# Kernel tuning notes

Measured on AMD Instinct MI355X. Metric: run time of the kernel, lower is better.

## Reference

```python
import jax, jax.numpy as jnp
import numpy as np
from jax import lax

HID = 768          # hidden_dim / embedding_dim
IN = 64            # input_dim = max_seq_length // num_heads
SEQ = 512          # max_seq_length
GROUPS = IN        # conv groups
BLUR_K = 5
BLUR_SIGMA = 1.0


def _gauss1d(k, sigma):
    half = (k - 1) * 0.5
    x = np.linspace(-half, half, k)
    pdf = np.exp(-0.5 * (x / sigma) ** 2)
    return pdf / pdf.sum()


def setup_inputs() -> dict:
    key = jax.random.key(0)
    ks = jax.random.split(key, 8)
    s = 0.02
    return {
        "inputs": jax.random.normal(ks[0], (16, SEQ, HID), jnp.float32),
        # Conv1d(768, 768, k=3, groups=64): weight [out_ch, in_ch/groups, k]
        "conv_w": jax.random.normal(ks[1], (HID, HID // GROUPS, 3), jnp.float32) * s,
        "conv_b": jnp.zeros((HID,), jnp.float32),
        "ln_g": jnp.ones((IN,), jnp.float32),
        "ln_b": jnp.zeros((IN,), jnp.float32),
        # function_info: Linear(64, 64), torch weight convention [out, in]
        "fi_w": jax.random.normal(ks[2], (IN, IN), jnp.float32) * s,
        "fi_b": jnp.zeros((IN,), jnp.float32),
        # block_info: Linear(64, 1)
        "bi_w": jax.random.normal(ks[3], (1, IN), jnp.float32) * s,
        "bi_b": jnp.zeros((1,), jnp.float32),
    }


def _forward(inputs, conv_w, conv_b, ln_g, ln_b, fi_w, fi_b, bi_w, bi_b):
    x = inputs.reshape(-1, HID, IN)  # [Bn, 768, 64] (raw row-major view, as torch .view)
    q = k = v = m = x

    # q: grouped Conv1d + residual, GELU, LayerNorm over last dim (64)
    qc = lax.conv_general_dilated(
        q, conv_w, window_strides=(1,), padding=[(1, 1)],
        feature_group_count=GROUPS, dimension_numbers=("NCH", "OIH", "NCH"))
    qc = qc + conv_b[None, :, None]
    q = jax.nn.gelu(qc + q, approximate=False)
    mu = jnp.mean(q, axis=-1, keepdims=True)
    var = jnp.mean(jnp.square(q - mu), axis=-1, keepdims=True)
    q = (q - mu) * lax.rsqrt(var + 1e-5) * ln_g + ln_b

    # v: Linear(64,64) + GELU
    v = jax.nn.gelu(v @ fi_w.T + fi_b, approximate=False)

    # k: dropout (eval -> identity), softmax over dim=-2 (channel axis), GELU
    k = jax.nn.gelu(jax.nn.softmax(k, axis=-2), approximate=False)

    # m: GaussianBlur(5, sigma fixed 1.0) over (H=768, W=64) with reflect pad, then Linear(64,1)
    g = _gauss1d(BLUR_K, BLUR_SIGMA)
    kern = jnp.asarray(np.outer(g, g), m.dtype)[None, None]  # [1,1,5,5]
    p = BLUR_K // 2
    mp = jnp.pad(m[:, None], ((0, 0), (0, 0), (p, p), (p, p)), mode="reflect")
    m = lax.conv_general_dilated(
        mp, kern, (1, 1), "VALID", dimension_numbers=("NCHW", "OIHW", "NCHW"))[:, 0]
    m = m @ bi_w.T + bi_b                        # [Bn, 768, 1]
    mask = jnp.broadcast_to(m, (m.shape[0], HID, HID))  # expand to [Bn,768,768]

    # SDPA: scale = 1/sqrt(E) with E = q.shape[-1] = 64; additive float mask
    scores = jnp.einsum("bce,bde->bcd", q, k) * (1.0 / np.sqrt(IN)) + mask
    attn = jax.nn.softmax(scores, axis=-1)
    out = jnp.einsum("bcd,bde->bce", attn, v)    # [Bn, 768, 64]
    return out.reshape(-1, SEQ, HID)


def reference(inputs, conv_w, conv_b, ln_g, ln_b, fi_w, fi_b, bi_w, bi_b):
    return _forward(inputs, conv_w, conv_b, ln_g, ln_b, fi_w, fi_b, bi_w, bi_b)
```

## Files before the change

### kernel.cpp

```cpp
#include <hip/hip_runtime.h>
#include <hip/hip_bf16.h>
#include <math.h>

#define NB 128
#define NC 768
#define NE 64
#define IPG 12

typedef __hip_bfloat16 bf16;
typedef __bf16 bf16v8 __attribute__((ext_vector_type(8)));
typedef __bf16 bf16v4 __attribute__((ext_vector_type(4)));
typedef __bf16 bf16v2 __attribute__((ext_vector_type(2)));
typedef float f32x4 __attribute__((ext_vector_type(4)));
typedef unsigned int u32;
typedef u32 u32x4 __attribute__((ext_vector_type(4)));

__device__ __forceinline__ float gelu_exact(float x) {
    return 0.5f * x * (1.0f + erff(x * 0.70710678118654752f));
}

#define MFMA16(a, b, c) __builtin_amdgcn_mfma_f32_16x16x32_bf16(a, b, c, 0, 0, 0)

__device__ __forceinline__ void gload_lds16(const void* g, void* l) {
    __builtin_amdgcn_global_load_lds(
        (const __attribute__((address_space(1))) void*)g,
        (__attribute__((address_space(3))) void*)l, 16, 0, 0);
}

__global__ __launch_bounds__(256) void k_stats(const float* __restrict__ x,
                                               float* __restrict__ sp) {
    int part = blockIdx.x, b = blockIdx.y;
    int e = threadIdx.x & 63, sub = threadIdx.x >> 6;
    const float* xb = x + (size_t)b * NC * NE + (size_t)(part * 96 + sub * 24) * NE;
    float s = 0.f;
    #pragma unroll
    for (int c = 0; c < 24; ++c) s += __expf(xb[c * NE + e]);
    __shared__ float red[4][64];
    red[sub][e] = s;
    __syncthreads();
    if (sub == 0)
        sp[(size_t)(b * 8 + part) * 64 + e] =
            red[0][e] + red[1][e] + red[2][e] + red[3][e];
}

__global__ __launch_bounds__(256) void k_conv(
    const float* __restrict__ x, const float* __restrict__ cw,
    const float* __restrict__ cb, const float* __restrict__ lg,
    const float* __restrict__ lb, bf16* __restrict__ qo)
{
    int b = blockIdx.x >> 4;
    int g = (blockIdx.x & 15) * 4 + (threadIdx.x >> 6);
    g = __builtin_amdgcn_readfirstlane(g);
    int h = threadIdx.x & 63;
    const float* xb = x + ((size_t)b * NC + g * IPG) * NE;

    float xi[IPG], xm[IPG], xp[IPG];
    #pragma unroll
    for (int i = 0; i < IPG; ++i) {
        xi[i] = xb[i * NE + h];
        float up = __shfl_up(xi[i], 1);
        float dn = __shfl_down(xi[i], 1);
        xm[i] = h ? up : 0.f;
        xp[i] = (h < 63) ? dn : 0.f;
    }
    float gam = lg[h], bet = lb[h];
    const float* wg = cw + (size_t)g * IPG * 36;

    for (int o = 0; o < IPG; ++o) {
        const float* wo = wg + o * 36;
        float acc = cb[g * IPG + o];
        #pragma unroll
        for (int i = 0; i < IPG; ++i)
            acc = fmaf(xm[i], wo[i*3], fmaf(xi[i], wo[i*3+1], fmaf(xp[i], wo[i*3+2], acc)));
        float gl = gelu_exact(acc + xi[o]);
        float s1 = gl, s2 = gl * gl;
        #pragma unroll
        for (int off = 32; off; off >>= 1) {
            s1 += __shfl_xor(s1, off);
            s2 += __shfl_xor(s2, off);
        }
        float mu  = s1 * (1.f / 64.f);
        float var = s2 * (1.f / 64.f) - mu * mu;
        float qn = (gl - mu) * rsqrtf(var + 1e-5f) * gam + bet;
        qo[((size_t)b * NC + g * IPG + o) * NE + h] = __float2bfloat16(qn * 0.125f);
    }
}

__global__ __launch_bounds__(256) void k_vk(
    const float* __restrict__ x, const float* __restrict__ fw,
    const float* __restrict__ fb, const float* __restrict__ sp,
    bf16* __restrict__ ko, bf16* __restrict__ vTo)
{
    int chunk = blockIdx.x, b = blockIdx.y;
    int tid = threadIdx.x, w = tid >> 6, l = tid & 63;
    int lr = l & 15, lc = (l >> 4) * 8;
    int rowb = chunk * 64 + w * 16;
    const float* xb = x + (size_t)b * NC * NE;

    __shared__ float sts[64];
    if (tid < 64) {
        float s = 0.f;
        #pragma unroll
        for (int p = 0; p < 8; ++p) s += sp[(size_t)(b * 8 + p) * 64 + tid];
        sts[tid] = 1.f / s;
    }

    bf16v8 bfr[4][2];
    float fbias[4];
    #pragma unroll
    for (int nt = 0; nt < 4; ++nt) {
        #pragma unroll
        for (int kt = 0; kt < 2; ++kt) {
            const float* p = fw + (nt*16 + lr) * 64 + kt*32 + lc;
            bf16v8 t;
            #pragma unroll
            for (int j = 0; j < 8; ++j) t[j] = (__bf16)p[j];
            bfr[nt][kt] = t;
        }
        fbias[nt] = fb[nt*16 + lr];
    }
    __syncthreads();

    float isA[8], isB[8];
    #pragma unroll
    for (int j = 0; j < 8; ++j) { isA[j] = sts[lc + j]; isB[j] = sts[32 + lc + j]; }

    const float* pa = xb + (size_t)(rowb + lr) * NE;
    float xa[8], xc[8];
    #pragma unroll
    for (int j = 0; j < 8; ++j) xa[j] = pa[lc + j];
    #pragma unroll
    for (int j = 0; j < 8; ++j) xc[j] = pa[32 + lc + j];

    bf16v8 a0, a1;
    #pragma unroll
    for (int j = 0; j < 8; ++j) a0[j] = (__bf16)xa[j];
    #pragma unroll
    for (int j = 0; j < 8; ++j) a1[j] = (__bf16)xc[j];

    bf16v8 kv0, kv1;
    #pragma unroll
    for (int j = 0; j < 8; ++j) kv0[j] = (__bf16)gelu_exact(__expf(xa[j]) * isA[j]);
    #pragma unroll
    for (int j = 0; j < 8; ++j) kv1[j] = (__bf16)gelu_exact(__expf(xc[j]) * isB[j]);
    bf16* kp = ko + ((size_t)b * NC + rowb + lr) * NE + lc;
    *(bf16v8*)kp = kv0;
    *(bf16v8*)(kp + 32) = kv1;

    #pragma unroll
    for (int nt = 0; nt < 4; ++nt) {
        f32x4 acc = {fbias[nt], fbias[nt], fbias[nt], fbias[nt]};
        acc = MFMA16(a0, bfr[nt][0], acc);
        acc = MFMA16(a1, bfr[nt][1], acc);
        bf16v4 pk;
        #pragma unroll
        for (int r = 0; r < 4; ++r) pk[r] = (__bf16)gelu_exact(acc[r]);
        int c = rowb + (l >> 4) * 4;
        *(bf16v4*)&vTo[((size_t)b * NE + nt*16 + lr) * NC + c] = pk;
    }
}

__device__ __forceinline__ bf16v8 softmax_exch(f32x4 s0, f32x4 s1, float& rsum,
                                               int srcA, int srcB, int hq) {
    float p0 = __expf(s0[0]), p1 = __expf(s0[1]), p2 = __expf(s0[2]), p3 = __expf(s0[3]);
    float p4 = __expf(s1[0]), p5 = __expf(s1[1]), p6 = __expf(s1[2]), p7 = __expf(s1[3]);
    rsum += ((p0 + p1) + (p2 + p3)) + ((p4 + p5) + (p6 + p7));
    bf16v2 t0; t0[0] = (__bf16)p0; t0[1] = (__bf16)p1;
    bf16v2 t1; t1[0] = (__bf16)p2; t1[1] = (__bf16)p3;
    bf16v2 t2; t2[0] = (__bf16)p4; t2[1] = (__bf16)p5;
    bf16v2 t3; t3[0] = (__bf16)p6; t3[1] = (__bf16)p7;
    u32 w0 = __builtin_bit_cast(u32, t0), w1 = __builtin_bit_cast(u32, t1);
    u32 w2 = __builtin_bit_cast(u32, t2), w3 = __builtin_bit_cast(u32, t3);
    u32 c0A = (u32)__shfl((int)w0, srcA), c1A = (u32)__shfl((int)w1, srcA);
    u32 c2A = (u32)__shfl((int)w2, srcA), c3A = (u32)__shfl((int)w3, srcA);
    u32 c0B = (u32)__shfl((int)w0, srcB), c1B = (u32)__shfl((int)w1, srcB);
    u32 c2B = (u32)__shfl((int)w2, srcB), c3B = (u32)__shfl((int)w3, srcB);
    u32x4 pau = { hq ? c2A : c0A, hq ? c3A : c1A,
                  hq ? c2B : c0B, hq ? c3B : c1B };
    return __builtin_bit_cast(bf16v8, pau);
}

__global__ __launch_bounds__(256, 2) void k_attn(const bf16* __restrict__ qb,
                                                 const bf16* __restrict__ kb,
                                                 const bf16* __restrict__ vT,
                                                 float* __restrict__ out) {
    __shared__ __align__(16) __bf16 ldsK[2][2048];
    __shared__ __align__(16) __bf16 ldsV[2][2048];

    int bid = blockIdx.x;
    int swz = (bid & 7) * 96 + (bid >> 3);
    int b = swz / 6, qt = swz - b * 6;
    int w = threadIdx.x >> 6, l = threadIdx.x & 63;
    int q0 = qt * 128 + w * 32;
    int lr = l & 15, hi = l >> 4;
    int hq = hi >> 1;
    int srcA = lr + ((hi & 1) << 5);
    int srcB = srcA + 16;

    int krow_ = w * 8 + (l >> 3);
    int kc16_ = (l & 7) ^ (l >> 3);
    const char* kgbase = (const char*)(kb + (size_t)b * NC * NE)
                       + krow_ * 128 + kc16_ * 16;
    int ve_   = w * 16 + (l >> 2);
    int vc16_ = (l & 3) ^ ((l >> 3) & 3);
    const char* vgbase = (const char*)(vT + (size_t)b * NE * NC)
                       + ve_ * 1536 + vc16_ * 16;

    int krd0 = lr * 64 + ((hi ^ (lr & 7)) << 3);
    int krd1 = lr * 64 + (((4 + hi) ^ (lr & 7)) << 3);
    int vsel = (lr >> 1) & 3;
    int vrd  = lr * 32 + ((hi ^ vsel) << 3);

    const bf16* qp = qb + ((size_t)b * NC + q0 + lr) * NE + hi * 8;
    bf16v8 qf00 = *(const bf16v8*)qp;
    bf16v8 qf01 = *(const bf16v8*)(qp + 32);
    bf16v8 qf10 = *(const bf16v8*)(qp + 16 * NE);
    bf16v8 qf11 = *(const bf16v8*)(qp + 16 * NE + 32);

    f32x4 o00 = {0,0,0,0}, o01 = {0,0,0,0}, o02 = {0,0,0,0}, o03 = {0,0,0,0};
    f32x4 o10 = {0,0,0,0}, o11 = {0,0,0,0}, o12 = {0,0,0,0}, o13 = {0,0,0,0};
    float rsum0 = 0.f, rsum1 = 0.f;

    gload_lds16(kgbase, &ldsK[0][w * 512]);
    gload_lds16(vgbase, &ldsV[0][w * 512]);
    __syncthreads();

    int cur = 0;
    for (int kt = 0; kt < 24; ++kt) {
        if (kt < 23) {
            gload_lds16(kgbase + (size_t)(kt + 1) * 4096, &ldsK[cur ^ 1][w * 512]);
            gload_lds16(vgbase + (size_t)(kt + 1) * 64,   &ldsV[cur ^ 1][w * 512]);
        }

        const __bf16* Kc = ldsK[cur];
        const __bf16* Vc = ldsV[cur];
        bf16v8 ka0 = *(const bf16v8*)&Kc[krd0];
        bf16v8 ka1 = *(const bf16v8*)&Kc[krd1];
        bf16v8 ka2 = *(const bf16v8*)&Kc[krd0 + 1024];
        bf16v8 ka3 = *(const bf16v8*)&Kc[krd1 + 1024];
        bf16v8 v0  = *(const bf16v8*)&Vc[vrd];
        bf16v8 v1  = *(const bf16v8*)&Vc[vrd + 512];
        bf16v8 v2  = *(const bf16v8*)&Vc[vrd + 1024];
        bf16v8 v3  = *(const bf16v8*)&Vc[vrd + 1536];

        f32x4 s00 = {0,0,0,0}, s01 = {0,0,0,0};
        s00 = MFMA16(ka0, qf00, s00);
        s00 = MFMA16(ka1, qf01, s00);
        s01 = MFMA16(ka2, qf00, s01);
        s01 = MFMA16(ka3, qf01, s01);
        f32x4 s10 = {0,0,0,0}, s11 = {0,0,0,0};
        s10 = MFMA16(ka0, qf10, s10);
        s10 = MFMA16(ka1, qf11, s10);
        s11 = MFMA16(ka2, qf10, s11);
        s11 = MFMA16(ka3, qf11, s11);

        bf16v8 pa0 = softmax_exch(s00, s01, rsum0, srcA, srcB, hq);
        bf16v8 pa1 = softmax_exch(s10, s11, rsum1, srcA, srcB, hq);

        o00 = MFMA16(pa0, v0, o00);
        o01 = MFMA16(pa0, v1, o01);
        o02 = MFMA16(pa0, v2, o02);
        o03 = MFMA16(pa0, v3, o03);
        o10 = MFMA16(pa1, v0, o10);
        o11 = MFMA16(pa1, v1, o11);
        o12 = MFMA16(pa1, v2, o12);
        o13 = MFMA16(pa1, v3, o13);

        __syncthreads();
        cur ^= 1;
    }

    rsum0 += __shfl_xor(rsum0, 16);
    rsum0 += __shfl_xor(rsum0, 32);
    rsum1 += __shfl_xor(rsum1, 16);
    rsum1 += __shfl_xor(rsum1, 32);
    float inv0 = 1.f / rsum0, inv1 = 1.f / rsum1;

    int qrow0 = q0 + hi * 4;
    #pragma unroll
    for (int r = 0; r < 4; ++r) {
        float iq = __shfl(inv0, hi * 4 + r);
        float* op = out + ((size_t)b * NC + qrow0 + r) * NE + lr;
        op[0]  = o00[r] * iq;
        op[16] = o01[r] * iq;
        op[32] = o02[r] * iq;
        op[48] = o03[r] * iq;
    }
    int qrow1 = q0 + 16 + hi * 4;
    #pragma unroll
    for (int r = 0; r < 4; ++r) {
        float iq = __shfl(inv1, hi * 4 + r);
        float* op = out + ((size_t)b * NC + qrow1 + r) * NE + lr;
        op[0]  = o10[r] * iq;
        op[16] = o11[r] * iq;
        op[32] = o12[r] * iq;
        op[48] = o13[r] * iq;
    }
}

extern "C" void kernel_launch(void* const* d_in, const int* in_sizes, int n_in,
                              void* d_out, int out_size, void* d_ws, size_t ws_size,
                              hipStream_t stream) {
    (void)in_sizes; (void)n_in; (void)out_size; (void)ws_size;
    const float* x      = (const float*)d_in[0];
    const float* conv_w = (const float*)d_in[1];
    const float* conv_b = (const float*)d_in[2];
    const float* ln_g   = (const float*)d_in[3];
    const float* ln_b   = (const float*)d_in[4];
    const float* fi_w   = (const float*)d_in[5];
    const float* fi_b   = (const float*)d_in[6];

    bf16* qbuf = (bf16*)d_ws;
    bf16* kbuf = qbuf + (size_t)NB * NC * NE;
    bf16* vT   = kbuf + (size_t)NB * NC * NE;
    float* stats = (float*)(vT + (size_t)NB * NC * NE);
    float* out = (float*)d_out;

    k_stats<<<dim3(8, NB), 256, 0, stream>>>(x, stats);
    k_conv<<<dim3(NB * 16), 256, 0, stream>>>(x, conv_w, conv_b, ln_g, ln_b, qbuf);
    k_vk<<<dim3(12, NB), 256, 0, stream>>>(x, fi_w, fi_b, stats, kbuf, vT);
    k_attn<<<dim3(768), 256, 0, stream>>>(qbuf, kbuf, vT, out);
}
```

Measured before the change: 85.85 us.

## Fuse conv, K/V projection and attention into one kernel with LDS-resident Q/K/V

Replaces the separate conv, K/V and attention kernels with a single 768-thread kernel per (batch, query-half). Each block computes its Q rows into LDS and rebuilds K and V for the whole batch in two 384-row halves, writing them to swizzled LDS instead of global bf16 buffers. This removes global round trips and two launches, but every batch's K and V are computed twice (once per query half), the grid shrinks to 256 large blocks, and the LDS footprint is about 144KB. It also swaps exact erf GELU for an Abramowitz-Stegun polynomial approximation and adds s_setprio around the MFMA groups.

Result: no change. 86.19 us (+0.4%).

```diff
diff --git a/kernel.cpp b/kernel.cpp
--- a/kernel.cpp
+++ b/kernel.cpp
@@ -16,16 +16,17 @@
 typedef u32 u32x4 __attribute__((ext_vector_type(4)));
 
 __device__ __forceinline__ float gelu_exact(float x) {
-    return 0.5f * x * (1.0f + erff(x * 0.70710678118654752f));
+    float ax = fabsf(x);
+    float t = __builtin_amdgcn_rcpf(fmaf(0.2316419f, ax, 1.0f));
+    float poly = t * fmaf(t, fmaf(t, fmaf(t, fmaf(t, 1.330274429f,
+                  -1.821255978f), 1.781477937f), -0.356563782f), 0.319381530f);
+    float pdf = 0.3989422804f * __expf(-0.5f * ax * ax);
+    float c = fmaf(-pdf, poly, 1.0f);
+    float cdf = (x >= 0.f) ? c : 1.0f - c;
+    return x * cdf;
 }
 
 #define MFMA16(a, b, c) __builtin_amdgcn_mfma_f32_16x16x32_bf16(a, b, c, 0, 0, 0)
-
-__device__ __forceinline__ void gload_lds16(const void* g, void* l) {
-    __builtin_amdgcn_global_load_lds(
-        (const __attribute__((address_space(1))) void*)g,
-        (__attribute__((address_space(3))) void*)l, 16, 0, 0);
-}
 
 __global__ __launch_bounds__(256) void k_stats(const float* __restrict__ x,
                                                float* __restrict__ sp) {
@@ -41,123 +42,6 @@
     if (sub == 0)
         sp[(size_t)(b * 8 + part) * 64 + e] =
             red[0][e] + red[1][e] + red[2][e] + red[3][e];
-}
-
-__global__ __launch_bounds__(256) void k_conv(
-    const float* __restrict__ x, const float* __restrict__ cw,
-    const float* __restrict__ cb, const float* __restrict__ lg,
-    const float* __restrict__ lb, bf16* __restrict__ qo)
-{
-    int b = blockIdx.x >> 4;
-    int g = (blockIdx.x & 15) * 4 + (threadIdx.x >> 6);
-    g = __builtin_amdgcn_readfirstlane(g);
-    int h = threadIdx.x & 63;
-    const float* xb = x + ((size_t)b * NC + g * IPG) * NE;
-
-    float xi[IPG], xm[IPG], xp[IPG];
-    #pragma unroll
-    for (int i = 0; i < IPG; ++i) {
-        xi[i] = xb[i * NE + h];
-        float up = __shfl_up(xi[i], 1);
-        float dn = __shfl_down(xi[i], 1);
-        xm[i] = h ? up : 0.f;
-        xp[i] = (h < 63) ? dn : 0.f;
-    }
-    float gam = lg[h], bet = lb[h];
-    const float* wg = cw + (size_t)g * IPG * 36;
-
-    for (int o = 0; o < IPG; ++o) {
-        const float* wo = wg + o * 36;
-        float acc = cb[g * IPG + o];
-        #pragma unroll
-        for (int i = 0; i < IPG; ++i)
-            acc = fmaf(xm[i], wo[i*3], fmaf(xi[i], wo[i*3+1], fmaf(xp[i], wo[i*3+2], acc)));
-        float gl = gelu_exact(acc + xi[o]);
-        float s1 = gl, s2 = gl * gl;
-        #pragma unroll
-        for (int off = 32; off; off >>= 1) {
-            s1 += __shfl_xor(s1, off);
-            s2 += __shfl_xor(s2, off);
-        }
-        float mu  = s1 * (1.f / 64.f);
-        float var = s2 * (1.f / 64.f) - mu * mu;
-        float qn = (gl - mu) * rsqrtf(var + 1e-5f) * gam + bet;
-        qo[((size_t)b * NC + g * IPG + o) * NE + h] = __float2bfloat16(qn * 0.125f);
-    }
-}
-
-__global__ __launch_bounds__(256) void k_vk(
-    const float* __restrict__ x, const float* __restrict__ fw,
-    const float* __restrict__ fb, const float* __restrict__ sp,
-    bf16* __restrict__ ko, bf16* __restrict__ vTo)
-{
-    int chunk = blockIdx.x, b = blockIdx.y;
-    int tid = threadIdx.x, w = tid >> 6, l = tid & 63;
-    int lr = l & 15, lc = (l >> 4) * 8;
-    int rowb = chunk * 64 + w * 16;
-    const float* xb = x + (size_t)b * NC * NE;
-
-    __shared__ float sts[64];
-    if (tid < 64) {
-        float s = 0.f;
-        #pragma unroll
-        for (int p = 0; p < 8; ++p) s += sp[(size_t)(b * 8 + p) * 64 + tid];
-        sts[tid] = 1.f / s;
-    }
-
-    bf16v8 bfr[4][2];
-    float fbias[4];
-    #pragma unroll
-    for (int nt = 0; nt < 4; ++nt) {
-        #pragma unroll
-        for (int kt = 0; kt < 2; ++kt) {
-            const float* p = fw + (nt*16 + lr) * 64 + kt*32 + lc;
-            bf16v8 t;
-            #pragma unroll
-            for (int j = 0; j < 8; ++j) t[j] = (__bf16)p[j];
-            bfr[nt][kt] = t;
-        }
-        fbias[nt] = fb[nt*16 + lr];
-    }
-    __syncthreads();
-
-    float isA[8], isB[8];
-    #pragma unroll
-    for (int j = 0; j < 8; ++j) { isA[j] = sts[lc + j]; isB[j] = sts[32 + lc + j]; }
-
-    const float* pa = xb + (size_t)(rowb + lr) * NE;
-    float xa[8], xc[8];
-    #pragma unroll
-    for (int j = 0; j < 8; ++j) xa[j] = pa[lc + j];
-    #pragma unroll
-    for (int j = 0; j < 8; ++j) xc[j] = pa[32 + lc + j];
-
-    bf16v8 a0, a1;
-    #pragma unroll
-    for (int j = 0; j < 8; ++j) a0[j] = (__bf16)xa[j];
-    #pragma unroll
-    for (int j = 0; j < 8; ++j) a1[j] = (__bf16)xc[j];
-
-    bf16v8 kv0, kv1;
-    #pragma unroll
-    for (int j = 0; j < 8; ++j) kv0[j] = (__bf16)gelu_exact(__expf(xa[j]) * isA[j]);
-    #pragma unroll
-    for (int j = 0; j < 8; ++j) kv1[j] = (__bf16)gelu_exact(__expf(xc[j]) * isB[j]);
-    bf16* kp = ko + ((size_t)b * NC + rowb + lr) * NE + lc;
-    *(bf16v8*)kp = kv0;
-    *(bf16v8*)(kp + 32) = kv1;
-
-    #pragma unroll
-    for (int nt = 0; nt < 4; ++nt) {
-        f32x4 acc = {fbias[nt], fbias[nt], fbias[nt], fbias[nt]};
-        acc = MFMA16(a0, bfr[nt][0], acc);
-        acc = MFMA16(a1, bfr[nt][1], acc);
-        bf16v4 pk;
-        #pragma unroll
-        for (int r = 0; r < 4; ++r) pk[r] = (__bf16)gelu_exact(acc[r]);
-        int c = rowb + (l >> 4) * 4;
-        *(bf16v4*)&vTo[((size_t)b * NE + nt*16 + lr) * NC + c] = pk;
-    }
 }
 
 __device__ __forceinline__ bf16v8 softmax_exch(f32x4 s0, f32x4 s1, float& rsum,
@@ -180,94 +64,199 @@
     return __builtin_bit_cast(bf16v8, pau);
 }
 
-__global__ __launch_bounds__(256, 2) void k_attn(const bf16* __restrict__ qb,
-                                                 const bf16* __restrict__ kb,
-                                                 const bf16* __restrict__ vT,
-                                                 float* __restrict__ out) {
-    __shared__ __align__(16) __bf16 ldsK[2][2048];
-    __shared__ __align__(16) __bf16 ldsV[2][2048];
+__global__ __launch_bounds__(768, 3) void k_fused(
+    const float* __restrict__ x, const float* __restrict__ cw,
+    const float* __restrict__ cb, const float* __restrict__ lg,
+    const float* __restrict__ lb, const float* __restrict__ fw,
+    const float* __restrict__ fb, const float* __restrict__ sp,
+    float* __restrict__ out)
+{
+    __shared__ __align__(16) __bf16 qlds[24576];
+    __shared__ __align__(16) __bf16 klds[24576];
+    __shared__ __align__(16) __bf16 vlds[24576];
+    __shared__ float stsL[64];
 
     int bid = blockIdx.x;
-    int swz = (bid & 7) * 96 + (bid >> 3);
-    int b = swz / 6, qt = swz - b * 6;
-    int w = threadIdx.x >> 6, l = threadIdx.x & 63;
-    int q0 = qt * 128 + w * 32;
+    int swz = (bid & 7) * 32 + (bid >> 3);
+    int b = swz >> 1, half_q = swz & 1;
+    int Q0 = half_q * 384;
+
+    int tid = threadIdx.x;
+    int w = tid >> 6, l = tid & 63;
+    const float* xb = x + (size_t)b * NC * NE;
+
+    if (tid < 64) {
+        float s = 0.f;
+        #pragma unroll
+        for (int p = 0; p < 8; ++p) s += sp[(size_t)(b * 8 + p) * 64 + tid];
+        stsL[tid] = 1.f / s;
+    }
+
+    {
+        int h = l;
+        float gam = lg[h], bet = lb[h];
+        for (int gg = w; gg < 32; gg += 12) {
+            int g = __builtin_amdgcn_readfirstlane(half_q * 32 + gg);
+            const float* xg = xb + (size_t)g * IPG * NE;
+            float xi[IPG], xm[IPG], xp[IPG];
+            #pragma unroll
+            for (int i = 0; i < IPG; ++i) {
+                xi[i] = xg[i * NE + h];
+                float up = __shfl_up(xi[i], 1);
+                float dn = __shfl_down(xi[i], 1);
+                xm[i] = h ? up : 0.f;
+                xp[i] = (h < 63) ? dn : 0.f;
+            }
+            const float* wg = cw + (size_t)g * IPG * 36;
+            for (int o = 0; o < IPG; ++o) {
+                const float* wo = wg + o * 36;
+                float acc = cb[g * IPG + o];
+                #pragma unroll
+                for (int i = 0; i < IPG; ++i)
+                    acc = fmaf(xm[i], wo[i*3], fmaf(xi[i], wo[i*3+1], fmaf(xp[i], wo[i*3+2], acc)));
+                float gl = gelu_exact(acc + xi[o]);
+                float s1 = gl, s2 = gl * gl;
+                #pragma unroll
+                for (int off = 32; off; off >>= 1) {
+                    s1 += __shfl_xor(s1, off);
+                    s2 += __shfl_xor(s2, off);
+                }
+                float mu  = s1 * (1.f / 64.f);
+                float var = s2 * (1.f / 64.f) - mu * mu;
+                float qn = (gl - mu) * rsqrtf(var + 1e-5f) * gam + bet;
+                int row = gg * 12 + o;
+                qlds[row * 64 + (((h >> 3) ^ (row & 7)) << 3) + (h & 7)] =
+                    (__bf16)(qn * 0.125f);
+            }
+        }
+    }
+    __syncthreads();
+
     int lr = l & 15, hi = l >> 4;
-    int hq = hi >> 1;
-    int srcA = lr + ((hi & 1) << 5);
-    int srcB = srcA + 16;
-
-    int krow_ = w * 8 + (l >> 3);
-    int kc16_ = (l & 7) ^ (l >> 3);
-    const char* kgbase = (const char*)(kb + (size_t)b * NC * NE)
-                       + krow_ * 128 + kc16_ * 16;
-    int ve_   = w * 16 + (l >> 2);
-    int vc16_ = (l & 3) ^ ((l >> 3) & 3);
-    const char* vgbase = (const char*)(vT + (size_t)b * NE * NC)
-                       + ve_ * 1536 + vc16_ * 16;
-
+    int hqx = hi >> 1;
+    int srcA = lr + ((hi & 1) << 5), srcB = srcA + 16;
     int krd0 = lr * 64 + ((hi ^ (lr & 7)) << 3);
     int krd1 = lr * 64 + (((4 + hi) ^ (lr & 7)) << 3);
     int vsel = (lr >> 1) & 3;
     int vrd  = lr * 32 + ((hi ^ vsel) << 3);
-
-    const bf16* qp = qb + ((size_t)b * NC + q0 + lr) * NE + hi * 8;
-    bf16v8 qf00 = *(const bf16v8*)qp;
-    bf16v8 qf01 = *(const bf16v8*)(qp + 32);
-    bf16v8 qf10 = *(const bf16v8*)(qp + 16 * NE);
-    bf16v8 qf11 = *(const bf16v8*)(qp + 16 * NE + 32);
+    int qbase = w * 2048;
+    bf16v8 qf00 = *(const bf16v8*)&qlds[qbase + krd0];
+    bf16v8 qf01 = *(const bf16v8*)&qlds[qbase + krd1];
+    bf16v8 qf10 = *(const bf16v8*)&qlds[qbase + 1024 + krd0];
+    bf16v8 qf11 = *(const bf16v8*)&qlds[qbase + 1024 + krd1];
 
     f32x4 o00 = {0,0,0,0}, o01 = {0,0,0,0}, o02 = {0,0,0,0}, o03 = {0,0,0,0};
     f32x4 o10 = {0,0,0,0}, o11 = {0,0,0,0}, o12 = {0,0,0,0}, o13 = {0,0,0,0};
     float rsum0 = 0.f, rsum1 = 0.f;
 
-    gload_lds16(kgbase, &ldsK[0][w * 512]);
-    gload_lds16(vgbase, &ldsV[0][w * 512]);
-    __syncthreads();
-
-    int cur = 0;
-    for (int kt = 0; kt < 24; ++kt) {
-        if (kt < 23) {
-            gload_lds16(kgbase + (size_t)(kt + 1) * 4096, &ldsK[cur ^ 1][w * 512]);
-            gload_lds16(vgbase + (size_t)(kt + 1) * 64,   &ldsV[cur ^ 1][w * 512]);
+    for (int hh = 0; hh < 2; ++hh) {
+        int R0 = hh * 384;
+
+        {
+            int lc = hi * 8;
+            float isA[8], isB[8];
+            #pragma unroll
+            for (int j = 0; j < 8; ++j) { isA[j] = stsL[lc + j]; isB[j] = stsL[32 + lc + j]; }
+            #pragma unroll
+            for (int ss = 0; ss < 2; ++ss) {
+                int r32 = ss * 16 + lr;
+                const float* pa = xb + (size_t)(R0 + w * 32 + r32) * NE;
+                bf16v8 kv0, kv1;
+                #pragma unroll
+                for (int j = 0; j < 8; ++j)
+                    kv0[j] = (__bf16)gelu_exact(__expf(pa[lc + j]) * isA[j]);
+                #pragma unroll
+                for (int j = 0; j < 8; ++j)
+                    kv1[j] = (__bf16)gelu_exact(__expf(pa[32 + lc + j]) * isB[j]);
+                int base = w * 2048 + r32 * 64;
+                *(bf16v8*)&klds[base + ((hi ^ (lr & 7)) << 3)]       = kv0;
+                *(bf16v8*)&klds[base + (((4 + hi) ^ (lr & 7)) << 3)] = kv1;
+            }
         }
 
-        const __bf16* Kc = ldsK[cur];
-        const __bf16* Vc = ldsV[cur];
-        bf16v8 ka0 = *(const bf16v8*)&Kc[krd0];
-        bf16v8 ka1 = *(const bf16v8*)&Kc[krd1];
-        bf16v8 ka2 = *(const bf16v8*)&Kc[krd0 + 1024];
-        bf16v8 ka3 = *(const bf16v8*)&Kc[krd1 + 1024];
-        bf16v8 v0  = *(const bf16v8*)&Vc[vrd];
-        bf16v8 v1  = *(const bf16v8*)&Vc[vrd + 512];
-        bf16v8 v2  = *(const bf16v8*)&Vc[vrd + 1024];
-        bf16v8 v3  = *(const bf16v8*)&Vc[vrd + 1536];
-
-        f32x4 s00 = {0,0,0,0}, s01 = {0,0,0,0};
-        s00 = MFMA16(ka0, qf00, s00);
-        s00 = MFMA16(ka1, qf01, s00);
-        s01 = MFMA16(ka2, qf00, s01);
-        s01 = MFMA16(ka3, qf01, s01);
-        f32x4 s10 = {0,0,0,0}, s11 = {0,0,0,0};
-        s10 = MFMA16(ka0, qf10, s10);
-        s10 = MFMA16(ka1, qf11, s10);
-        s11 = MFMA16(ka2, qf10, s11);
-        s11 = MFMA16(ka3, qf11, s11);
-
-        bf16v8 pa0 = softmax_exch(s00, s01, rsum0, srcA, srcB, hq);
-        bf16v8 pa1 = softmax_exch(s10, s11, rsum1, srcA, srcB, hq);
-
-        o00 = MFMA16(pa0, v0, o00);
-        o01 = MFMA16(pa0, v1, o01);
-        o02 = MFMA16(pa0, v2, o02);
-        o03 = MFMA16(pa0, v3, o03);
-        o10 = MFMA16(pa1, v0, o10);
-        o11 = MFMA16(pa1, v1, o11);
-        o12 = MFMA16(pa1, v2, o12);
-        o13 = MFMA16(pa1, v3, o13);
-
+        {
+            bf16v8 bfr[4][2];
+            float fbias[4];
+            #pragma unroll
+            for (int nt = 0; nt < 4; ++nt) {
+                #pragma unroll
+                for (int kt = 0; kt < 2; ++kt) {
+                    const float* p = fw + (nt*16 + lr) * 64 + kt*32 + (hi * 8);
+                    bf16v8 t;
+                    #pragma unroll
+                    for (int j = 0; j < 8; ++j) t[j] = (__bf16)p[j];
+                    bfr[nt][kt] = t;
+                }
+                fbias[nt] = fb[nt*16 + lr];
+            }
+            #pragma unroll
+            for (int tt = 0; tt < 2; ++tt) {
+                int t16 = w * 2 + tt;
+                const float* pa = xb + (size_t)(R0 + t16 * 16 + lr) * NE + hi * 8;
+                bf16v8 a0, a1;
+                #pragma unroll
+                for (int j = 0; j < 8; ++j) a0[j] = (__bf16)pa[j];
+                #pragma unroll
+                for (int j = 0; j < 8; ++j) a1[j] = (__bf16)pa[32 + j];
+                int tile = t16 >> 1;
+                int kchunk = (t16 & 1) * 2 + (hi >> 1);
+                int kin = (hi & 1) * 4;
+                #pragma unroll
+                for (int nt = 0; nt < 4; ++nt) {
+                    f32x4 acc = {fbias[nt], fbias[nt], fbias[nt], fbias[nt]};
+                    acc = MFMA16(a0, bfr[nt][0], acc);
+                    acc = MFMA16(a1, bfr[nt][1], acc);
+                    bf16v4 pk;
+                    #pragma unroll
+                    for (int r = 0; r < 4; ++r) pk[r] = (__bf16)gelu_exact(acc[r]);
+                    int e = nt * 16 + lr;
+                    *(bf16v4*)&vlds[tile * 2048 + e * 32 +
+                        ((kchunk ^ ((lr >> 1) & 3)) << 3) + kin] = pk;
+                }
+            }
+        }
         __syncthreads();
-        cur ^= 1;
+
+        for (int t = 0; t < 12; ++t) {
+            const __bf16* Kc = &klds[t * 2048];
+            const __bf16* Vc = &vlds[t * 2048];
+            bf16v8 ka0 = *(const bf16v8*)&Kc[krd0];
+            bf16v8 ka1 = *(const bf16v8*)&Kc[krd1];
+            bf16v8 ka2 = *(const bf16v8*)&Kc[krd0 + 1024];
+            bf16v8 ka3 = *(const bf16v8*)&Kc[krd1 + 1024];
+            bf16v8 v0  = *(const bf16v8*)&Vc[vrd];
+            bf16v8 v1  = *(const bf16v8*)&Vc[vrd + 512];
+            bf16v8 v2  = *(const bf16v8*)&Vc[vrd + 1024];
+            bf16v8 v3  = *(const bf16v8*)&Vc[vrd + 1536];
+
+            __builtin_amdgcn_s_setprio(1);
+            f32x4 s00 = {0,0,0,0}, s01 = {0,0,0,0};
+            s00 = MFMA16(ka0, qf00, s00);
+            s00 = MFMA16(ka1, qf01, s00);
+            s01 = MFMA16(ka2, qf00, s01);
+            s01 = MFMA16(ka3, qf01, s01);
+            f32x4 s10 = {0,0,0,0}, s11 = {0,0,0,0};
+            s10 = MFMA16(ka0, qf10, s10);
+            s10 = MFMA16(ka1, qf11, s10);
+            s11 = MFMA16(ka2, qf10, s11);
+            s11 = MFMA16(ka3, qf11, s11);
+            __builtin_amdgcn_s_setprio(0);
+
+            bf16v8 pa0 = softmax_exch(s00, s01, rsum0, srcA, srcB, hqx);
+            bf16v8 pa1 = softmax_exch(s10, s11, rsum1, srcA, srcB, hqx);
+
+            __builtin_amdgcn_s_setprio(1);
+            o00 = MFMA16(pa0, v0, o00);
+            o01 = MFMA16(pa0, v1, o01);
+            o02 = MFMA16(pa0, v2, o02);
+            o03 = MFMA16(pa0, v3, o03);
+            o10 = MFMA16(pa1, v0, o10);
+            o11 = MFMA16(pa1, v1, o11);
+            o12 = MFMA16(pa1, v2, o12);
+            o13 = MFMA16(pa1, v3, o13);
+            __builtin_amdgcn_s_setprio(0);
+        }
+        __syncthreads();
     }
 
     rsum0 += __shfl_xor(rsum0, 16);
@@ -276,7 +265,8 @@
     rsum1 += __shfl_xor(rsum1, 32);
     float inv0 = 1.f / rsum0, inv1 = 1.f / rsum1;
 
-    int qrow0 = q0 + hi * 4;
+    int q0g = Q0 + w * 32;
+    int qrow0 = q0g + hi * 4;
     #pragma unroll
     for (int r = 0; r < 4; ++r) {
         float iq = __shfl(inv0, hi * 4 + r);
@@ -286,7 +276,7 @@
         op[32] = o02[r] * iq;
         op[48] = o03[r] * iq;
     }
-    int qrow1 = q0 + 16 + hi * 4;
+    int qrow1 = q0g + 16 + hi * 4;
     #pragma unroll
     for (int r = 0; r < 4; ++r) {
         float iq = __shfl(inv1, hi * 4 + r);
@@ -310,14 +300,10 @@
     const float* fi_w   = (const float*)d_in[5];
     const float* fi_b   = (const float*)d_in[6];
 
-    bf16* qbuf = (bf16*)d_ws;
-    bf16* kbuf = qbuf + (size_t)NB * NC * NE;
-    bf16* vT   = kbuf + (size_t)NB * NC * NE;
-    float* stats = (float*)(vT + (size_t)NB * NC * NE);
+    float* stats = (float*)d_ws;
     float* out = (float*)d_out;
 
     k_stats<<<dim3(8, NB), 256, 0, stream>>>(x, stats);
-    k_conv<<<dim3(NB * 16), 256, 0, stream>>>(x, conv_w, conv_b, ln_g, ln_b, qbuf);
-    k_vk<<<dim3(12, NB), 256, 0, stream>>>(x, fi_w, fi_b, stats, kbuf, vT);
-    k_attn<<<dim3(768), 256, 0, stream>>>(qbuf, kbuf, vT, out);
-}
+    k_fused<<<dim3(256), 768, 0, stream>>>(x, conv_w, conv_b, ln_g, ln_b,
+                                           fi_w, fi_b, stats, out);
+}
```
